# Kernel optimization log

Hardware: AMD Instinct MI355X
Metric: run time of the kernel (lower is better)

The kernel has to match this reference:

```python
import jax, jax.numpy as jnp
import numpy as np
from jax import lax

EPS = 1e-6
CLAMP = 1e4


def _ln_last(x, w, b):
    # fp32 LayerNorm over last dim
    mu = jnp.mean(x, axis=-1, keepdims=True)
    var = jnp.mean(jnp.square(x - mu), axis=-1, keepdims=True)
    return (x - mu) * lax.rsqrt(var + EPS) * w + b


def _nan_clean(x):
    return jnp.nan_to_num(x, nan=0.0, posinf=CLAMP, neginf=-CLAMP)


def setup_inputs() -> dict:
    key = jax.random.key(0)
    B, C, H, W = 4, 256, 64, 64
    hid = 2 * C  # expand=2
    k = 3        # d_conv
    ks = jax.random.split(key, 12)
    s = 0.02
    return {
        "x": jax.random.normal(ks[0], (B, C, H, W), jnp.float32),
        "ln2d_w": jnp.ones((C,), jnp.float32),
        "ln2d_b": jnp.zeros((C,), jnp.float32),
        "inproj_w": jax.random.normal(ks[1], (C, C), jnp.float32) * s,
        "inproj_b": jnp.zeros((C,), jnp.float32),
        "dw2d_w": jax.random.normal(ks[2], (C, 3, 3), jnp.float32) * s,
        "dw2d_b": jnp.zeros((C,), jnp.float32),
        "ssm_ln_w": jnp.ones((C,), jnp.float32),
        "ssm_ln_b": jnp.zeros((C,), jnp.float32),
        "ssm_in_w": jax.random.normal(ks[3], (2 * hid, C), jnp.float32) * s,
        "ssm_in_b": jnp.zeros((2 * hid,), jnp.float32),
        "ssm_dw_w": jax.random.normal(ks[4], (hid, k), jnp.float32) * s,
        "ssm_dw_b": jnp.zeros((hid,), jnp.float32),
        "ssm_out_w": jax.random.normal(ks[5], (C, hid), jnp.float32) * s,
        "ssm_out_b": jnp.zeros((C,), jnp.float32),
        "outproj_w": jax.random.normal(ks[6], (C, C), jnp.float32) * s,
        "outproj_b": jnp.zeros((C,), jnp.float32),
    }


def reference(x, ln2d_w, ln2d_b, inproj_w, inproj_b, dw2d_w, dw2d_b,
              ssm_ln_w, ssm_ln_b, ssm_in_w, ssm_in_b, ssm_dw_w, ssm_dw_b,
              ssm_out_w, ssm_out_b, outproj_w, outproj_b):
    B, C, H, W = x.shape
    L = H * W

    # LN2d over channel dim (per-pixel LN on C)
    y = _ln_last(x.transpose(0, 2, 3, 1), ln2d_w, ln2d_b).transpose(0, 3, 1, 2)

    # 1x1 conv in_proj
    y = jnp.einsum('bchw,oc->bohw', y, inproj_w) + inproj_b[None, :, None, None]

    # depthwise 3x3 conv, SAME padding
    y = lax.conv_general_dilated(
        y, dw2d_w[:, None, :, :], (1, 1), ((1, 1), (1, 1)),
        dimension_numbers=('NCHW', 'OIHW', 'NCHW'),
        feature_group_count=C) + dw2d_b[None, :, None, None]

    # cross-scan: 4 routes (B,L,C)
    s0 = y.reshape(B, C, L).transpose(0, 2, 1)                      # row-major
    s1 = s0[:, ::-1]                                                # reversed
    s2 = y.transpose(0, 1, 3, 2).reshape(B, C, L).transpose(0, 2, 1)  # col-major
    s3 = s2[:, ::-1]
    s = jnp.concatenate([s0, s1, s2, s3], axis=0)  # (4B, L, C), shared SSM weights

    # MambaOrLite fallback: LN -> GLU -> depthwise conv1d -> out proj + residual
    r = _ln_last(s, ssm_ln_w, ssm_ln_b)
    r = r @ ssm_in_w.T + ssm_in_b                   # (4B, L, 2*hid)
    a, g = jnp.split(r, 2, axis=-1)
    r = a * jax.nn.sigmoid(g)                       # (4B, L, hid)
    r = r.transpose(0, 2, 1)                        # (4B, hid, L)
    hid = r.shape[1]
    k = ssm_dw_w.shape[-1]
    pad = ((k - 1) // 2, k // 2)
    r = lax.conv_general_dilated(
        r, ssm_dw_w[:, None, :], (1,), (pad,),
        dimension_numbers=('NCH', 'OIH', 'NCH'),
        feature_group_count=hid) + ssm_dw_b[None, :, None]
    r = r.transpose(0, 2, 1) @ ssm_out_w.T + ssm_out_b  # (4B, L, C)
    ys = _nan_clean(r) + s

    # cross-merge: average the 4 routes back to (B,C,H,W)
    y0, y1, y2, y3 = jnp.split(ys, 4, axis=0)
    m0 = y0.transpose(0, 2, 1).reshape(B, C, H, W)
    m1 = y1[:, ::-1].transpose(0, 2, 1).reshape(B, C, H, W)
    m2 = y2.transpose(0, 2, 1).reshape(B, C, W, H).transpose(0, 1, 3, 2)
    m3 = y3[:, ::-1].transpose(0, 2, 1).reshape(B, C, W, H).transpose(0, 1, 3, 2)
    m = (m0 + m1 + m2 + m3) * 0.25

    out = jnp.einsum('bchw,oc->bohw', m, outproj_w) + outproj_b[None, :, None, None]
    out = _nan_clean(out)
    return out + x
```

## Files before the change

### kernel.cpp

```cpp
#include <hip/hip_runtime.h>

typedef float f32x4 __attribute__((ext_vector_type(4)));
typedef __bf16 bf16x8 __attribute__((ext_vector_type(8)));
typedef unsigned short u16;
typedef unsigned int u32;

__device__ __forceinline__ float bf2f(u32 b) {
  u32 x = (b & 0xffffu) << 16;
  return __builtin_bit_cast(float, x);
}
__device__ __forceinline__ u16 f2bf(float f) {
  u32 x = __builtin_bit_cast(u32, f);
  x += 0x7fffu + ((x >> 16) & 1u);
  return (u16)(x >> 16);
}
__device__ __forceinline__ void gload16(const void* g, void* l) {
  __builtin_amdgcn_global_load_lds((__attribute__((address_space(1))) void*)g,
                                   (__attribute__((address_space(3))) void*)l,
                                   16, 0, 0);
}

__global__ __launch_bounds__(256, 2)
void k_ln2d_prep(const float* __restrict__ x, const float* __restrict__ lw,
                 const float* __restrict__ lb, u16* __restrict__ A,
                 const float* __restrict__ inproj_w, const float* __restrict__ ssm_in_w,
                 const float* __restrict__ ssm_out_w, const float* __restrict__ outproj_w,
                 const float* __restrict__ dw2d_w, const float* __restrict__ ssm_dw_w,
                 const float* __restrict__ ssm_dw_b, const float* __restrict__ ssm_out_b,
                 u16* __restrict__ w1b, u16* __restrict__ w2b, u16* __restrict__ w3b,
                 u16* __restrict__ w4b, float* __restrict__ cvec, float* __restrict__ wT9,
                 float* __restrict__ w02, float* __restrict__ w14) {
  __shared__ float T[256 * 65];
  __shared__ float ps1[4][64], ps2[4][64];
  __shared__ float mu[64], rsd[64];
  int bid = blockIdx.x, tid = threadIdx.x;
  if (bid >= 256) {
    int pb = bid - 256;
    if (pb < 512) {
      const float* s; u16* d; int base;
      if (pb < 256)      { s = ssm_in_w;  d = w2b; base = pb; }
      else if (pb < 384) { s = ssm_out_w; d = w3b; base = pb - 256; }
      else if (pb < 448) { s = inproj_w;  d = w1b; base = pb - 384; }
      else               { s = outproj_w; d = w4b; base = pb - 448; }
      int i = base * 1024 + tid * 4;
      float4 v = *(const float4*)&s[i];
      u32 a = (u32)f2bf(v.x) | ((u32)f2bf(v.y) << 16);
      u32 b = (u32)f2bf(v.z) | ((u32)f2bf(v.w) << 16);
      *(uint2*)&d[i] = make_uint2(a, b);
    } else if (pb == 512) {
      float s = ssm_out_b[tid];
      const float* wr = ssm_out_w + (size_t)tid * 512;
      #pragma unroll 8
      for (int k = 0; k < 512; ++k) s += ssm_dw_b[k] * wr[k];
      cvec[tid] = s;
    } else {
      #pragma unroll
      for (int j = 0; j < 9; ++j) wT9[j * 256 + tid] = dw2d_w[tid * 9 + j];
      #pragma unroll
      for (int q = 0; q < 2; ++q) {
        int c = tid + q * 256;
        w02[c] = ssm_dw_w[c * 3 + 0] + ssm_dw_w[c * 3 + 2];
        w14[c] = 4.f * ssm_dw_w[c * 3 + 1];
      }
    }
    return;
  }
  int wv = tid >> 6, lane = tid & 63;
  int cq = lane >> 4, p4 = (lane & 15) * 4;
  int n0 = bid * 64, bb = n0 >> 12, hw0 = n0 & 4095;
  const float* xb = x + ((size_t)bb << 20);
  float s0 = 0, s1 = 0, s2 = 0, s3 = 0;
  float q0 = 0, q1 = 0, q2 = 0, q3 = 0;
  #pragma unroll 4
  for (int i = 0; i < 16; ++i) {
    int c = wv * 64 + i * 4 + cq;
    float4 v = *(const float4*)&xb[((size_t)c << 12) + hw0 + p4];
    T[c * 65 + p4 + 0] = v.x; T[c * 65 + p4 + 1] = v.y;
    T[c * 65 + p4 + 2] = v.z; T[c * 65 + p4 + 3] = v.w;
    s0 += v.x; s1 += v.y; s2 += v.z; s3 += v.w;
    q0 += v.x * v.x; q1 += v.y * v.y; q2 += v.z * v.z; q3 += v.w * v.w;
  }
  #pragma unroll
  for (int off = 16; off < 64; off <<= 1) {
    s0 += __shfl_xor(s0, off); s1 += __shfl_xor(s1, off);
    s2 += __shfl_xor(s2, off); s3 += __shfl_xor(s3, off);
    q0 += __shfl_xor(q0, off); q1 += __shfl_xor(q1, off);
    q2 += __shfl_xor(q2, off); q3 += __shfl_xor(q3, off);
  }
  if (cq == 0) {
    ps1[wv][p4 + 0] = s0; ps1[wv][p4 + 1] = s1; ps1[wv][p4 + 2] = s2; ps1[wv][p4 + 3] = s3;
    ps2[wv][p4 + 0] = q0; ps2[wv][p4 + 1] = q1; ps2[wv][p4 + 2] = q2; ps2[wv][p4 + 3] = q3;
  }
  __syncthreads();
  if (tid < 64) {
    float S1 = ps1[0][tid] + ps1[1][tid] + ps1[2][tid] + ps1[3][tid];
    float S2 = ps2[0][tid] + ps2[1][tid] + ps2[2][tid] + ps2[3][tid];
    float m = S1 * (1.f / 256.f);
    float var = S2 * (1.f / 256.f) - m * m;
    mu[tid] = m;
    rsd[tid] = rsqrtf(var + 1e-6f);
  }
  __syncthreads();
  int c4b = (tid & 15) * 4, p2b = tid >> 4;
  #pragma unroll
  for (int cc = 0; cc < 4; ++cc) {
    int c4 = cc * 64 + c4b;
    float4 w4 = *(const float4*)&lw[c4];
    float4 g4 = *(const float4*)&lb[c4];
    #pragma unroll
    for (int i2 = 0; i2 < 4; ++i2) {
      int p2 = p2b + 16 * i2;
      float m = mu[p2], rs = rsd[p2];
      float o0 = (T[(c4 + 0) * 65 + p2] - m) * rs * w4.x + g4.x;
      float o1 = (T[(c4 + 1) * 65 + p2] - m) * rs * w4.y + g4.y;
      float o2 = (T[(c4 + 2) * 65 + p2] - m) * rs * w4.z + g4.z;
      float o3 = (T[(c4 + 3) * 65 + p2] - m) * rs * w4.w + g4.w;
      u32 a = (u32)f2bf(o0) | ((u32)f2bf(o1) << 16);
      u32 b = (u32)f2bf(o2) | ((u32)f2bf(o3) << 16);
      *(uint2*)&A[(size_t)(n0 + p2) * 256 + c4] = make_uint2(a, b);
    }
  }
}

__global__ __launch_bounds__(256)
void k_dw3x3_ln(const u16* __restrict__ Y1, const float* __restrict__ wT,
                const float* __restrict__ dwb, const float* __restrict__ lnw,
                const float* __restrict__ lnb, u16* __restrict__ Yc,
                u16* __restrict__ A) {
  int tid = threadIdx.x;
  int n = blockIdx.x * 4 + (tid >> 6);
  int lane = tid & 63;
  int c0 = lane * 4;
  int b = n >> 12, hw = n & 4095, h = hw >> 6, w = hw & 63;
  float4 b4 = *(const float4*)&dwb[c0];
  float a0 = b4.x, a1 = b4.y, a2 = b4.z, a3 = b4.w;
  #pragma unroll
  for (int ky = 0; ky < 3; ++ky) {
    int hh = h + ky - 1;
    if (hh < 0 || hh > 63) continue;
    #pragma unroll
    for (int kx = 0; kx < 3; ++kx) {
      int ww = w + kx - 1;
      if (ww < 0 || ww > 63) continue;
      size_t nn = ((size_t)b << 12) + (hh << 6) + ww;
      uint2 u = *(const uint2*)&Y1[nn * 256 + c0];
      float4 w4 = *(const float4*)&wT[(ky * 3 + kx) * 256 + c0];
      a0 += bf2f(u.x) * w4.x;
      a1 += bf2f(u.x >> 16) * w4.y;
      a2 += bf2f(u.y) * w4.z;
      a3 += bf2f(u.y >> 16) * w4.w;
    }
  }
  u32 p0 = (u32)f2bf(a0) | ((u32)f2bf(a1) << 16);
  u32 p1 = (u32)f2bf(a2) | ((u32)f2bf(a3) << 16);
  *(uint2*)&Yc[(size_t)n * 256 + c0] = make_uint2(p0, p1);
  float s1 = a0 + a1 + a2 + a3;
  float s2 = a0 * a0 + a1 * a1 + a2 * a2 + a3 * a3;
  #pragma unroll
  for (int off = 1; off < 64; off <<= 1) {
    s1 += __shfl_xor(s1, off);
    s2 += __shfl_xor(s2, off);
  }
  float m = s1 * (1.f / 256.f);
  float var = s2 * (1.f / 256.f) - m * m;
  float rs = rsqrtf(var + 1e-6f);
  float4 w4 = *(const float4*)&lnw[c0];
  float4 g4 = *(const float4*)&lnb[c0];
  float o0 = (a0 - m) * rs * w4.x + g4.x;
  float o1 = (a1 - m) * rs * w4.y + g4.y;
  float o2 = (a2 - m) * rs * w4.z + g4.z;
  float o3 = (a3 - m) * rs * w4.w + g4.w;
  u32 qa = (u32)f2bf(o0) | ((u32)f2bf(o1) << 16);
  u32 qb = (u32)f2bf(o2) | ((u32)f2bf(o3) << 16);
  *(uint2*)&A[(size_t)n * 256 + c0] = make_uint2(qa, qb);
}

template <int EPI>
__global__ __launch_bounds__(256, 4)
void k_gemm2(const u16* __restrict__ R, const u16* __restrict__ Cm,
             const float* __restrict__ bias, int K, int nCt, int ldo,
             u16* __restrict__ outb, float* __restrict__ outf,
             const float* __restrict__ resf) {
  __shared__ u16 tR[2][64 * 32];
  __shared__ u16 tC[2][128 * 32];
  int tid = threadIdx.x, lane = tid & 63, wv = tid >> 6;
  int rt = blockIdx.x / nCt, ct = blockIdx.x % nCt;
  int r0 = rt * 64, c0 = ct * 128;
  int fr = lane & 15, kc = lane >> 4;
  int sr = lane >> 2, sc = (lane & 3) * 8;
  f32x4 acc[4][2] = {};
  int nK = K >> 5;
  const u16* gR  = R  + (size_t)(r0 + wv * 16 + sr) * K + sc;
  const u16* gC0 = Cm + (size_t)(c0 + wv * 32 + sr) * K + sc;
  const u16* gC1 = Cm + (size_t)(c0 + wv * 32 + 16 + sr) * K + sc;
  auto STAGE = [&](int buf, int kt) {
    int k0 = kt * 32;
    gload16(gR + k0,  &tR[buf][wv * 16 * 32]);
    gload16(gC0 + k0, &tC[buf][(wv * 32) * 32]);
    gload16(gC1 + k0, &tC[buf][(wv * 32 + 16) * 32]);
  };
  auto COMPUTE = [&](int buf) {
    bf16x8 af[4], wf[2];
    #pragma unroll
    for (int m = 0; m < 4; ++m)
      af[m] = *(const bf16x8*)&tR[buf][(m * 16 + fr) * 32 + kc * 8];
    #pragma unroll
    for (int n = 0; n < 2; ++n)
      wf[n] = *(const bf16x8*)&tC[buf][(wv * 32 + n * 16 + fr) * 32 + kc * 8];
    #pragma unroll
    for (int m = 0; m < 4; ++m)
      #pragma unroll
      for (int n = 0; n < 2; ++n)
        acc[m][n] = __builtin_amdgcn_mfma_f32_16x16x32_bf16(af[m], wf[n], acc[m][n], 0, 0, 0);
  };
  STAGE(0, 0);
  __syncthreads();
  int cur = 0;
  for (int kt = 0; kt < nK - 1; ++kt) {
    STAGE(cur ^ 1, kt + 1);
    __builtin_amdgcn_sched_barrier(0);
    COMPUTE(cur);
    __syncthreads();
    cur ^= 1;
  }
  COMPUTE(cur);
  #pragma unroll
  for (int m = 0; m < 4; ++m) {
    #pragma unroll
    for (int n = 0; n < 2; ++n) {
      #pragma unroll
      for (int r = 0; r < 4; ++r) {
        float v = acc[m][n][r];
        if (EPI == 0) {
          int gn = r0 + m * 16 + kc * 4 + r;
          int go = c0 + wv * 32 + n * 16 + fr;
          outb[(size_t)gn * ldo + go] = f2bf(v + bias[go]);
        } else {
          int go = r0 + m * 16 + kc * 4 + r;
          int gn = c0 + wv * 32 + n * 16 + fr;
          int b = gn >> 12, hw = gn & 4095;
          size_t idx = (((size_t)(b * 256 + go)) << 12) + hw;
          outf[idx] = v + bias[go] + resf[idx];
        }
      }
    }
  }
}

__global__ __launch_bounds__(256, 3)
void k_gate2(const u16* __restrict__ A, const u16* __restrict__ W,
             const float* __restrict__ bias, u16* __restrict__ G) {
  __shared__ u16 tR[2][64 * 32];
  __shared__ u16 tCa[2][128 * 32];
  __shared__ u16 tCg[2][128 * 32];
  int tid = threadIdx.x, lane = tid & 63, wv = tid >> 6;
  int rt = blockIdx.x >> 2, ot = blockIdx.x & 3;
  int r0 = rt * 64, o0 = ot * 128;
  int fr = lane & 15, kc = lane >> 4;
  int sr = lane >> 2, sc = (lane & 3) * 8;
  const int K = 256;
  f32x4 acca[4][2] = {}, accg[4][2] = {};
  const u16* gR  = A + (size_t)(r0 + wv * 16 + sr) * K + sc;
  const u16* gA0 = W + (size_t)(o0 + wv * 32 + sr) * K + sc;
  const u16* gA1 = W + (size_t)(o0 + wv * 32 + 16 + sr) * K + sc;
  const u16* gG0 = W + (size_t)(512 + o0 + wv * 32 + sr) * K + sc;
  const u16* gG1 = W + (size_t)(512 + o0 + wv * 32 + 16 + sr) * K + sc;
  auto STAGE = [&](int buf, int kt) {
    int k0 = kt * 32;
    gload16(gR + k0,  &tR[buf][wv * 16 * 32]);
    gload16(gA0 + k0, &tCa[buf][(wv * 32) * 32]);
    gload16(gA1 + k0, &tCa[buf][(wv * 32 + 16) * 32]);
    gload16(gG0 + k0, &tCg[buf][(wv * 32) * 32]);
    gload16(gG1 + k0, &tCg[buf][(wv * 32 + 16) * 32]);
  };
  auto COMPUTE = [&](int buf) {
    bf16x8 af[4], wa[2], wg[2];
    #pragma unroll
    for (int m = 0; m < 4; ++m)
      af[m] = *(const bf16x8*)&tR[buf][(m * 16 + fr) * 32 + kc * 8];
    #pragma unroll
    for (int n = 0; n < 2; ++n) {
      wa[n] = *(const bf16x8*)&tCa[buf][(wv * 32 + n * 16 + fr) * 32 + kc * 8];
      wg[n] = *(const bf16x8*)&tCg[buf][(wv * 32 + n * 16 + fr) * 32 + kc * 8];
    }
    #pragma unroll
    for (int m = 0; m < 4; ++m)
      #pragma unroll
      for (int n = 0; n < 2; ++n) {
        acca[m][n] = __builtin_amdgcn_mfma_f32_16x16x32_bf16(af[m], wa[n], acca[m][n], 0, 0, 0);
        accg[m][n] = __builtin_amdgcn_mfma_f32_16x16x32_bf16(af[m], wg[n], accg[m][n], 0, 0, 0);
      }
  };
  STAGE(0, 0);
  __syncthreads();
  int cur = 0;
  for (int kt = 0; kt < 7; ++kt) {
    STAGE(cur ^ 1, kt + 1);
    __builtin_amdgcn_sched_barrier(0);
    COMPUTE(cur);
    __syncthreads();
    cur ^= 1;
  }
  COMPUTE(cur);
  #pragma unroll
  for (int m = 0; m < 4; ++m) {
    #pragma unroll
    for (int n = 0; n < 2; ++n) {
      #pragma unroll
      for (int r = 0; r < 4; ++r) {
        int gn = r0 + m * 16 + kc * 4 + r;
        int go = o0 + wv * 32 + n * 16 + fr;
        float a = acca[m][n][r] + bias[go];
        float g = accg[m][n][r] + bias[512 + go];
        G[(size_t)gn * 512 + go] = f2bf(a / (1.f + expf(-g)));
      }
    }
  }
}

__global__ __launch_bounds__(256, 2)
void k_gemm_scan(const u16* __restrict__ G, const u16* __restrict__ W3,
                 const float* __restrict__ w02, const float* __restrict__ w14,
                 const float* __restrict__ cvec, const u16* __restrict__ Yc,
                 u16* __restrict__ M) {
  __shared__ u16 tR[2][32 * 32];
  __shared__ u16 tC[2][256 * 32];
  int tid = threadIdx.x, lane = tid & 63, wv = tid >> 6;
  int r0 = blockIdx.x * 32;
  int fr = lane & 15, kc = lane >> 4;
  int zrow = tid >> 3;
  int zg = (tid & 7) * 4;
  int n = r0 + zrow;
  int b = n >> 12, hw = n & 4095, h = hw >> 6, w = hw & 63;
  int m = w * 64 + h;
  int mm1 = m - 1, mp1 = m + 1;
  size_t o_c = (size_t)n * 512 + zg;
  size_t o_p = (size_t)(hw > 0 ? n - 1 : n) * 512 + zg;
  size_t o_n = (size_t)(hw < 4095 ? n + 1 : n) * 512 + zg;
  size_t o_u = (size_t)(m > 0 ? ((b << 12) + ((mm1 & 63) << 6) + (mm1 >> 6)) : n) * 512 + zg;
  size_t o_d = (size_t)(m < 4095 ? ((b << 12) + ((mp1 & 63) << 6) + (mp1 >> 6)) : n) * 512 + zg;
  float mP = hw > 0 ? 1.f : 0.f, mN = hw < 4095 ? 1.f : 0.f;
  float mU = m > 0 ? 1.f : 0.f, mD = m < 4095 ? 1.f : 0.f;
  f32x4 acc[2][4] = {};
  auto STAGE_C = [&](int buf, int kt) {
    int k0 = kt * 32;
    #pragma unroll
    for (int i = 0; i < 4; ++i) {
      int s0 = wv * 256 + i * 64;
      int s = s0 + lane;
      int row = s >> 2, off = (s & 3) * 8;
      gload16(W3 + (size_t)row * 512 + k0 + off, &tC[buf][s0 * 8]);
    }
  };
  uint2 lc, lp, ln_, lu, ld;
  float4 va, vb;
  auto ZLOAD = [&](int kt) {
    int c = kt * 32 + zg;
    lc = *(const uint2*)&G[o_c + (kt * 32)];
    lp = *(const uint2*)&G[o_p + (kt * 32)];
    ln_ = *(const uint2*)&G[o_n + (kt * 32)];
    lu = *(const uint2*)&G[o_u + (kt * 32)];
    ld = *(const uint2*)&G[o_d + (kt * 32)];
    va = *(const float4*)&w02[c];
    vb = *(const float4*)&w14[c];
  };
  auto ZSTORE = [&](int buf) {
    float s_0 = mP * bf2f(lp.x) + mN * bf2f(ln_.x) + mU * bf2f(lu.x) + mD * bf2f(ld.x);
    float s_1 = mP * bf2f(lp.x >> 16) + mN * bf2f(ln_.x >> 16) + mU * bf2f(lu.x >> 16) + mD * bf2f(ld.x >> 16);
    float s_2 = mP * bf2f(lp.y) + mN * bf2f(ln_.y) + mU * bf2f(lu.y) + mD * bf2f(ld.y);
    float s_3 = mP * bf2f(lp.y >> 16) + mN * bf2f(ln_.y >> 16) + mU * bf2f(lu.y >> 16) + mD * bf2f(ld.y >> 16);
    float z0 = va.x * s_0 + vb.x * bf2f(lc.x);
    float z1 = va.y * s_1 + vb.y * bf2f(lc.x >> 16);
    float z2 = va.z * s_2 + vb.z * bf2f(lc.y);
    float z3 = va.w * s_3 + vb.w * bf2f(lc.y >> 16);
    u32 p0 = (u32)f2bf(z0) | ((u32)f2bf(z1) << 16);
    u32 p1 = (u32)f2bf(z2) | ((u32)f2bf(z3) << 16);
    *(uint2*)&tR[buf][zrow * 32 + zg] = make_uint2(p0, p1);
  };
  auto COMPUTE = [&](int buf) {
    bf16x8 af[2], wf[4];
    #pragma unroll
    for (int mi = 0; mi < 2; ++mi)
      af[mi] = *(const bf16x8*)&tR[buf][(mi * 16 + fr) * 32 + kc * 8];
    #pragma unroll
    for (int ni = 0; ni < 4; ++ni)
      wf[ni] = *(const bf16x8*)&tC[buf][(wv * 64 + ni * 16 + fr) * 32 + kc * 8];
    #pragma unroll
    for (int mi = 0; mi < 2; ++mi)
      #pragma unroll
      for (int ni = 0; ni < 4; ++ni)
        acc[mi][ni] = __builtin_amdgcn_mfma_f32_16x16x32_bf16(af[mi], wf[ni], acc[mi][ni], 0, 0, 0);
  };
  STAGE_C(0, 0);
  ZLOAD(0);
  ZSTORE(0);
  __syncthreads();
  int cur = 0;
  for (int kt = 0; kt < 15; ++kt) {
    ZLOAD(kt + 1);
    STAGE_C(cur ^ 1, kt + 1);
    COMPUTE(cur);
    ZSTORE(cur ^ 1);
    __syncthreads();
    cur ^= 1;
  }
  COMPUTE(cur);
  #pragma unroll
  for (int mi = 0; mi < 2; ++mi) {
    #pragma unroll
    for (int ni = 0; ni < 4; ++ni) {
      #pragma unroll
      for (int r = 0; r < 4; ++r) {
        int gn = r0 + mi * 16 + kc * 4 + r;
        int go = wv * 64 + ni * 16 + fr;
        size_t idx = (size_t)gn * 256 + go;
        M[idx] = f2bf(0.25f * acc[mi][ni][r] + cvec[go] + bf2f(Yc[idx]));
      }
    }
  }
}

extern "C" void kernel_launch(void* const* d_in, const int* in_sizes, int n_in,
                              void* d_out, int out_size, void* d_ws, size_t ws_size,
                              hipStream_t stream) {
  const float* x         = (const float*)d_in[0];
  const float* ln2d_w    = (const float*)d_in[1];
  const float* ln2d_b    = (const float*)d_in[2];
  const float* inproj_w  = (const float*)d_in[3];
  const float* inproj_b  = (const float*)d_in[4];
  const float* dw2d_w    = (const float*)d_in[5];
  const float* dw2d_b    = (const float*)d_in[6];
  const float* ssm_ln_w  = (const float*)d_in[7];
  const float* ssm_ln_b  = (const float*)d_in[8];
  const float* ssm_in_w  = (const float*)d_in[9];
  const float* ssm_in_b  = (const float*)d_in[10];
  const float* ssm_dw_w  = (const float*)d_in[11];
  const float* ssm_dw_b  = (const float*)d_in[12];
  const float* ssm_out_w = (const float*)d_in[13];
  const float* ssm_out_b = (const float*)d_in[14];
  const float* outproj_w = (const float*)d_in[15];
  const float* outproj_b = (const float*)d_in[16];
  float* out = (float*)d_out;

  char* ws = (char*)d_ws;
  size_t off = 0;
  auto take = [&](size_t bytes) -> char* {
    char* p = ws + off;
    off = (off + bytes + 255) & ~(size_t)255;
    return p;
  };
  u16* w1b    = (u16*)take(65536 * 2);
  u16* w2b    = (u16*)take(262144 * 2);
  u16* w3b    = (u16*)take(131072 * 2);
  u16* w4b    = (u16*)take(65536 * 2);
  float* cvec = (float*)take(256 * 4);
  float* wT9  = (float*)take(9 * 256 * 4);
  float* w02  = (float*)take(512 * 4);
  float* w14  = (float*)take(512 * 4);
  u16* Abuf   = (u16*)take((size_t)16384 * 256 * 2);
  u16* Y1     = (u16*)take((size_t)16384 * 256 * 2);
  u16* Yc     = (u16*)take((size_t)16384 * 256 * 2);
  u16* G      = (u16*)take((size_t)16384 * 512 * 2);
  (void)ws_size; (void)in_sizes; (void)n_in; (void)out_size;

  k_ln2d_prep<<<770, 256, 0, stream>>>(x, ln2d_w, ln2d_b, Abuf,
                                       inproj_w, ssm_in_w, ssm_out_w, outproj_w,
                                       dw2d_w, ssm_dw_w, ssm_dw_b, ssm_out_b,
                                       w1b, w2b, w3b, w4b, cvec, wT9, w02, w14);
  k_gemm2<0><<<512, 256, 0, stream>>>(Abuf, w1b, inproj_b, 256, 2, 256,
                                      Y1, nullptr, nullptr);
  k_dw3x3_ln<<<4096, 256, 0, stream>>>(Y1, wT9, dw2d_b, ssm_ln_w, ssm_ln_b, Yc, Abuf);
  k_gate2<<<1024, 256, 0, stream>>>(Abuf, w2b, ssm_in_b, G);
  k_gemm_scan<<<512, 256, 0, stream>>>(G, w3b, w02, w14, cvec, Yc, Abuf);
  k_gemm2<2><<<512, 256, 0, stream>>>(w4b, Abuf, outproj_b, 256, 128, 0,
                                      nullptr, out, x);
}
```

Measured before the change: 105.7 us.

## Add XCD-aware block swizzle, enlarge gate GEMM tile, nontemporal epilogue loads

Adds an XCD swizzle so consecutive logical tiles land on the same chiplet in the dwconv, gemm, gate and scan kernels, improving L2 locality. The gate GEMM tile grows from 64x128 to 128x128 on a 2x2 wave layout, halving the grid and reusing weight tiles across more rows, at the cost of more registers and lower occupancy. The output-projection GEMM now walks row tiles fastest and uses nontemporal loads and stores for the residual and output. Compile-time tile counts replace runtime division.

```diff
diff --git a/kernel.cpp b/kernel.cpp
--- a/kernel.cpp
+++ b/kernel.cpp
@@ -18,6 +18,10 @@
   __builtin_amdgcn_global_load_lds((__attribute__((address_space(1))) void*)g,
                                    (__attribute__((address_space(3))) void*)l,
                                    16, 0, 0);
+}
+__device__ __forceinline__ int xcd_swz(int bid, int nwg) {
+  int per = nwg >> 3;
+  return (bid & 7) * per + (bid >> 3);
 }
 
 __global__ __launch_bounds__(256, 2)
@@ -128,7 +132,8 @@
                 const float* __restrict__ lnb, u16* __restrict__ Yc,
                 u16* __restrict__ A) {
   int tid = threadIdx.x;
-  int n = blockIdx.x * 4 + (tid >> 6);
+  int wg = xcd_swz(blockIdx.x, 4096);
+  int n = wg * 4 + (tid >> 6);
   int lane = tid & 63;
   int c0 = lane * 4;
   int b = n >> 12, hw = n & 4095, h = hw >> 6, w = hw & 63;
@@ -175,16 +180,19 @@
   *(uint2*)&A[(size_t)n * 256 + c0] = make_uint2(qa, qb);
 }
 
-template <int EPI>
+template <int EPI, int NCT, bool RFAST>
 __global__ __launch_bounds__(256, 4)
 void k_gemm2(const u16* __restrict__ R, const u16* __restrict__ Cm,
-             const float* __restrict__ bias, int K, int nCt, int ldo,
+             const float* __restrict__ bias, int K, int ldo,
              u16* __restrict__ outb, float* __restrict__ outf,
              const float* __restrict__ resf) {
   __shared__ u16 tR[2][64 * 32];
   __shared__ u16 tC[2][128 * 32];
   int tid = threadIdx.x, lane = tid & 63, wv = tid >> 6;
-  int rt = blockIdx.x / nCt, ct = blockIdx.x % nCt;
+  int wg = xcd_swz(blockIdx.x, gridDim.x);
+  int nRt = gridDim.x / NCT;
+  int rt = RFAST ? (wg % nRt) : (wg / NCT);
+  int ct = RFAST ? (wg / nRt) : (wg % NCT);
   int r0 = rt * 64, c0 = ct * 128;
   int fr = lane & 15, kc = lane >> 4;
   int sr = lane >> 2, sc = (lane & 3) * 8;
@@ -240,55 +248,56 @@
           int gn = c0 + wv * 32 + n * 16 + fr;
           int b = gn >> 12, hw = gn & 4095;
           size_t idx = (((size_t)(b * 256 + go)) << 12) + hw;
-          outf[idx] = v + bias[go] + resf[idx];
+          float res = __builtin_nontemporal_load(&resf[idx]);
+          __builtin_nontemporal_store(v + bias[go] + res, &outf[idx]);
         }
       }
     }
   }
 }
 
-__global__ __launch_bounds__(256, 3)
+__global__ __launch_bounds__(256, 2)
 void k_gate2(const u16* __restrict__ A, const u16* __restrict__ W,
              const float* __restrict__ bias, u16* __restrict__ G) {
-  __shared__ u16 tR[2][64 * 32];
+  __shared__ u16 tR[2][128 * 32];
   __shared__ u16 tCa[2][128 * 32];
   __shared__ u16 tCg[2][128 * 32];
   int tid = threadIdx.x, lane = tid & 63, wv = tid >> 6;
-  int rt = blockIdx.x >> 2, ot = blockIdx.x & 3;
-  int r0 = rt * 64, o0 = ot * 128;
+  int wg = xcd_swz(blockIdx.x, 512);
+  int rt = wg >> 2, ot = wg & 3;
+  int r0 = rt * 128, o0 = ot * 128;
+  int wr = wv >> 1, wc = wv & 1;
   int fr = lane & 15, kc = lane >> 4;
-  int sr = lane >> 2, sc = (lane & 3) * 8;
   const int K = 256;
-  f32x4 acca[4][2] = {}, accg[4][2] = {};
-  const u16* gR  = A + (size_t)(r0 + wv * 16 + sr) * K + sc;
-  const u16* gA0 = W + (size_t)(o0 + wv * 32 + sr) * K + sc;
-  const u16* gA1 = W + (size_t)(o0 + wv * 32 + 16 + sr) * K + sc;
-  const u16* gG0 = W + (size_t)(512 + o0 + wv * 32 + sr) * K + sc;
-  const u16* gG1 = W + (size_t)(512 + o0 + wv * 32 + 16 + sr) * K + sc;
+  f32x4 acca[4][4] = {}, accg[4][4] = {};
   auto STAGE = [&](int buf, int kt) {
     int k0 = kt * 32;
-    gload16(gR + k0,  &tR[buf][wv * 16 * 32]);
-    gload16(gA0 + k0, &tCa[buf][(wv * 32) * 32]);
-    gload16(gA1 + k0, &tCa[buf][(wv * 32 + 16) * 32]);
-    gload16(gG0 + k0, &tCg[buf][(wv * 32) * 32]);
-    gload16(gG1 + k0, &tCg[buf][(wv * 32 + 16) * 32]);
+    #pragma unroll
+    for (int i = 0; i < 2; ++i) {
+      int s0 = wv * 128 + i * 64;
+      int s = s0 + lane;
+      int row = s >> 2, off = (s & 3) * 8;
+      gload16(A + (size_t)(r0 + row) * K + k0 + off, &tR[buf][s0 * 8]);
+      gload16(W + (size_t)(o0 + row) * K + k0 + off, &tCa[buf][s0 * 8]);
+      gload16(W + (size_t)(512 + o0 + row) * K + k0 + off, &tCg[buf][s0 * 8]);
+    }
   };
   auto COMPUTE = [&](int buf) {
-    bf16x8 af[4], wa[2], wg[2];
+    bf16x8 af[4], wa[4], wgf[4];
     #pragma unroll
     for (int m = 0; m < 4; ++m)
-      af[m] = *(const bf16x8*)&tR[buf][(m * 16 + fr) * 32 + kc * 8];
-    #pragma unroll
-    for (int n = 0; n < 2; ++n) {
-      wa[n] = *(const bf16x8*)&tCa[buf][(wv * 32 + n * 16 + fr) * 32 + kc * 8];
-      wg[n] = *(const bf16x8*)&tCg[buf][(wv * 32 + n * 16 + fr) * 32 + kc * 8];
+      af[m] = *(const bf16x8*)&tR[buf][(wr * 64 + m * 16 + fr) * 32 + kc * 8];
+    #pragma unroll
+    for (int n = 0; n < 4; ++n) {
+      wa[n]  = *(const bf16x8*)&tCa[buf][(wc * 64 + n * 16 + fr) * 32 + kc * 8];
+      wgf[n] = *(const bf16x8*)&tCg[buf][(wc * 64 + n * 16 + fr) * 32 + kc * 8];
     }
     #pragma unroll
     for (int m = 0; m < 4; ++m)
       #pragma unroll
-      for (int n = 0; n < 2; ++n) {
+      for (int n = 0; n < 4; ++n) {
         acca[m][n] = __builtin_amdgcn_mfma_f32_16x16x32_bf16(af[m], wa[n], acca[m][n], 0, 0, 0);
-        accg[m][n] = __builtin_amdgcn_mfma_f32_16x16x32_bf16(af[m], wg[n], accg[m][n], 0, 0, 0);
+        accg[m][n] = __builtin_amdgcn_mfma_f32_16x16x32_bf16(af[m], wgf[n], accg[m][n], 0, 0, 0);
       }
   };
   STAGE(0, 0);
@@ -305,11 +314,11 @@
   #pragma unroll
   for (int m = 0; m < 4; ++m) {
     #pragma unroll
-    for (int n = 0; n < 2; ++n) {
+    for (int n = 0; n < 4; ++n) {
       #pragma unroll
       for (int r = 0; r < 4; ++r) {
-        int gn = r0 + m * 16 + kc * 4 + r;
-        int go = o0 + wv * 32 + n * 16 + fr;
+        int gn = r0 + wr * 64 + m * 16 + kc * 4 + r;
+        int go = o0 + wc * 64 + n * 16 + fr;
         float a = acca[m][n][r] + bias[go];
         float g = accg[m][n][r] + bias[512 + go];
         G[(size_t)gn * 512 + go] = f2bf(a / (1.f + expf(-g)));
@@ -326,7 +335,8 @@
   __shared__ u16 tR[2][32 * 32];
   __shared__ u16 tC[2][256 * 32];
   int tid = threadIdx.x, lane = tid & 63, wv = tid >> 6;
-  int r0 = blockIdx.x * 32;
+  int wg = xcd_swz(blockIdx.x, 512);
+  int r0 = wg * 32;
   int fr = lane & 15, kc = lane >> 4;
   int zrow = tid >> 3;
   int zg = (tid & 7) * 4;
@@ -356,11 +366,11 @@
   float4 va, vb;
   auto ZLOAD = [&](int kt) {
     int c = kt * 32 + zg;
-    lc = *(const uint2*)&G[o_c + (kt * 32)];
-    lp = *(const uint2*)&G[o_p + (kt * 32)];
+    lc  = *(const uint2*)&G[o_c + (kt * 32)];
+    lp  = *(const uint2*)&G[o_p + (kt * 32)];
     ln_ = *(const uint2*)&G[o_n + (kt * 32)];
-    lu = *(const uint2*)&G[o_u + (kt * 32)];
-    ld = *(const uint2*)&G[o_d + (kt * 32)];
+    lu  = *(const uint2*)&G[o_u + (kt * 32)];
+    ld  = *(const uint2*)&G[o_d + (kt * 32)];
     va = *(const float4*)&w02[c];
     vb = *(const float4*)&w14[c];
   };
@@ -467,11 +477,11 @@
                                        inproj_w, ssm_in_w, ssm_out_w, outproj_w,
                                        dw2d_w, ssm_dw_w, ssm_dw_b, ssm_out_b,
                                        w1b, w2b, w3b, w4b, cvec, wT9, w02, w14);
-  k_gemm2<0><<<512, 256, 0, stream>>>(Abuf, w1b, inproj_b, 256, 2, 256,
-                                      Y1, nullptr, nullptr);
+  k_gemm2<0, 2, false><<<512, 256, 0, stream>>>(Abuf, w1b, inproj_b, 256, 256,
+                                                Y1, nullptr, nullptr);
   k_dw3x3_ln<<<4096, 256, 0, stream>>>(Y1, wT9, dw2d_b, ssm_ln_w, ssm_ln_b, Yc, Abuf);
-  k_gate2<<<1024, 256, 0, stream>>>(Abuf, w2b, ssm_in_b, G);
+  k_gate2<<<512, 256, 0, stream>>>(Abuf, w2b, ssm_in_b, G);
   k_gemm_scan<<<512, 256, 0, stream>>>(G, w3b, w02, w14, cvec, Yc, Abuf);
-  k_gemm2<2><<<512, 256, 0, stream>>>(w4b, Abuf, outproj_b, 256, 128, 0,
-                                      nullptr, out, x);
-}
+  k_gemm2<2, 128, true><<<512, 256, 0, stream>>>(w4b, Abuf, outproj_b, 256, 0,
+                                                 nullptr, out, x);
+}
```

After: 108.4 us. 2.6% more time.
